# Kernel tuning notes

Measured on AMD Instinct MI355X. Metric: run time of the kernel, lower is better.

The kernel has to match this reference:

```python
import math
import jax, jax.numpy as jnp
import numpy as np

NUM_HEADS = 16


def setup_inputs() -> dict:
    key = jax.random.key(0)
    ks = jax.random.split(key, 5)
    B, S, D = 2, 2048, 1024
    return {
        "x": jax.random.normal(ks[0], (B, S, D), dtype=jnp.float32),
        "w_in": jax.random.normal(ks[1], (3 * D, D), dtype=jnp.float32) * (1.0 / math.sqrt(D)),
        "b_in": jax.random.normal(ks[2], (3 * D,), dtype=jnp.float32) * 0.02,
        "w_out": jax.random.normal(ks[3], (D, D), dtype=jnp.float32) * (1.0 / math.sqrt(D)),
        "b_out": jax.random.normal(ks[4], (D,), dtype=jnp.float32) * 0.02,
        "causal_mask": 1,
    }


def reference(x, w_in, b_in, w_out, b_out, causal_mask):
    B, S, D = x.shape
    H = NUM_HEADS
    dh = D // H
    # in-projection: torch Linear -> x @ W^T + b, then chunk into q,k,v
    qkv = x @ w_in.T + b_in                      # [B,S,3D]
    q, k, v = jnp.split(qkv, 3, axis=-1)         # each [B,S,D]
    q = q.reshape(B, S, H, dh).transpose(0, 2, 1, 3)  # [B,H,S,dh]
    k = k.reshape(B, S, H, dh).transpose(0, 2, 1, 3)
    v = v.reshape(B, S, H, dh).transpose(0, 2, 1, 3)
    # NOTE: original computes k @ q^T => scores indexed [key, query]
    scores = jnp.einsum("bhkd,bhqd->bhkq", k, q) / math.sqrt(dh)  # [B,H,Sk,Sq]
    if causal_mask:
        # triu(1) on the [k,q] matrix: mask where q_index > k_index
        mask = jnp.triu(jnp.ones((S, S), dtype=bool), 1)
        scores = jnp.where(mask, -jnp.inf, scores)
    att = jax.nn.softmax(scores, axis=-1)        # softmax over query axis (faithful)
    out = jnp.einsum("bhkq,bhqd->bhkd", att, v)  # [B,H,S,dh]
    out = out.transpose(0, 2, 1, 3).reshape(B, S, D)
    return out @ w_out.T + b_out
```

## Files before the change

kernel.cpp:

```cpp
#include <hip/hip_runtime.h>

typedef unsigned short u16;
typedef short bfrag __attribute__((ext_vector_type(8)));
typedef float facc  __attribute__((ext_vector_type(4)));
typedef float f16x  __attribute__((ext_vector_type(16)));

__device__ __forceinline__ u16 f2bf(float f){
  union { float f; unsigned u; } v; v.f = f;
  unsigned r = v.u + 0x7fffu + ((v.u >> 16) & 1u);
  return (u16)(r >> 16);
}

__device__ __forceinline__ unsigned cvt_pk_bf16(float lo, float hi){
  unsigned d;
  asm("v_cvt_pk_bf16_f32 %0, %1, %2" : "=v"(d) : "v"(lo), "v"(hi));
  return d;
}

__device__ __forceinline__ void gl_lds16(const void* g, void* l){
  __builtin_amdgcn_global_load_lds(
      (const __attribute__((address_space(1))) unsigned int*)g,
      (__attribute__((address_space(3))) unsigned int*)l,
      16, 0, 0);
}

__global__ __launch_bounds__(256) void cvt3_kernel(
    const float* __restrict__ s0, u16* __restrict__ d0, int n0,
    const float* __restrict__ s1, u16* __restrict__ d1, int n1,
    const float* __restrict__ s2, u16* __restrict__ d2)
{
  int i = (blockIdx.x * 256 + threadIdx.x) * 4;
  const float* src; u16* dst;
  if (i < n0){ src = s0; dst = d0; }
  else if (i < n0 + n1){ src = s1; dst = d1; i -= n0; }
  else { src = s2; dst = d2; i -= n0 + n1; }
  float4 f = *(const float4*)(src + i);
  ushort4 o;
  o.x = f2bf(f.x); o.y = f2bf(f.y); o.z = f2bf(f.z); o.w = f2bf(f.w);
  *(ushort4*)(dst + i) = o;
}

__device__ __forceinline__ void stage_tile(const u16* __restrict__ G, u16* lds,
                                           int row0, int k0, int K, int tid){
  #pragma unroll
  for (int c = 0; c < 2; ++c){
    int e = c * 2048 + tid * 8;
    int row = e >> 5, col = e & 31;
    gl_lds16(G + (size_t)(row0 + row) * K + k0 + col, lds + c * 2048 + (tid >> 6) * 512);
  }
}

template<int EPI>
__global__ __launch_bounds__(256) void gemm_bt(
    const u16* __restrict__ A, const u16* __restrict__ B,
    const float* __restrict__ bias, float* __restrict__ Cf,
    u16* __restrict__ qkv, int M, int N, int K)
{
  __shared__ u16 smem[16384];
  u16* Ash = smem;
  u16* Bsh = smem + 8192;
  const int tid = threadIdx.x, lane = tid & 63;
  const int w = tid >> 6, wm = w >> 1, wn = w & 1;
  const int cl = lane & 15, g8 = (lane >> 4) * 8;

  constexpr int NW = (EPI == 1) ? 12 : 4;
  const int bid = blockIdx.x;
  const int chunk = bid & 7, pos = bid >> 3;
  const int mt = (chunk >> 1) * 8 + pos / NW;
  const int nt = (chunk & 1) * NW + pos % NW;
  const int n0 = nt * 128, m0 = mt * 128;

  facc acc[4][4];
  #pragma unroll
  for (int mi = 0; mi < 4; ++mi)
    #pragma unroll
    for (int ni = 0; ni < 4; ++ni)
      acc[mi][ni] = (facc){0.f, 0.f, 0.f, 0.f};

  const int NT = K >> 5;
  stage_tile(A, Ash, m0, 0, K, tid);
  stage_tile(B, Bsh, n0, 0, K, tid);
  __syncthreads();
  int cur = 0;
  for (int kt = 0; kt < NT; ++kt){
    if (kt + 1 < NT){
      stage_tile(A, Ash + (cur ^ 1) * 4096, m0, (kt + 1) << 5, K, tid);
      stage_tile(B, Bsh + (cur ^ 1) * 4096, n0, (kt + 1) << 5, K, tid);
    }
    const u16* As = Ash + cur * 4096; const u16* Bs = Bsh + cur * 4096;
    bfrag af[4], bfr[4];
    #pragma unroll
    for (int mi = 0; mi < 4; ++mi)
      af[mi] = *(const bfrag*)&As[(wm * 64 + mi * 16 + cl) * 32 + g8];
    #pragma unroll
    for (int ni = 0; ni < 4; ++ni)
      bfr[ni] = *(const bfrag*)&Bs[(wn * 64 + ni * 16 + cl) * 32 + g8];
    #pragma unroll
    for (int mi = 0; mi < 4; ++mi)
      #pragma unroll
      for (int ni = 0; ni < 4; ++ni)
        acc[mi][ni] = __builtin_amdgcn_mfma_f32_16x16x32_bf16(af[mi], bfr[ni], acc[mi][ni], 0, 0, 0);
    __syncthreads();
    cur ^= 1;
  }

  const int r0 = (lane >> 4) * 4;
  const bool isv = (EPI == 1) && (n0 >= 2048);

  if (!isv){
    #pragma unroll
    for (int mi = 0; mi < 4; ++mi){
      const int mbase = m0 + wm * 64 + mi * 16 + r0;
      #pragma unroll
      for (int ni = 0; ni < 4; ++ni){
        const int n = n0 + wn * 64 + ni * 16 + cl;
        const float bv = bias[n];
        #pragma unroll
        for (int j = 0; j < 4; ++j){
          float v = acc[mi][ni][j] + bv;
          const int mm = mbase + j;
          if (EPI == 0){
            Cf[(size_t)mm * N + n] = v;
          } else {
            const int part = n >> 10, rest = n & 1023;
            const int h = rest >> 6, d = rest & 63;
            const int bb = mm >> 11, s = mm & 2047;
            if (part == 0) v *= 0.18033688011112042f;
            qkv[(size_t)part * 4194304 + (size_t)((bb * 16 + h) * 2048 + s) * 64 + d] = f2bf(v);
          }
        }
      }
    }
  } else {
    u16* tr = smem;
    const int bb = m0 >> 11;
    const int s0 = m0 & 2047;
    const int h0 = (n0 - 2048) >> 6;
    u16* vt_base = qkv + (size_t)2 * 4194304;
    const int trow = tid >> 2, tq = tid & 3;
    #pragma unroll
    for (int p = 0; p < 2; ++p){
      __syncthreads();
      if (wn == p){
        #pragma unroll
        for (int mi = 0; mi < 4; ++mi){
          const int sl = wm * 64 + mi * 16 + r0;
          #pragma unroll
          for (int ni = 0; ni < 4; ++ni){
            const int i = ni * 16 + cl;
            const float bv = bias[n0 + p * 64 + i];
            #pragma unroll
            for (int j = 0; j < 4; ++j)
              tr[i * 132 + sl + j] = f2bf(acc[mi][ni][j] + bv);
          }
        }
      }
      __syncthreads();
      u16* dst = vt_base + (size_t)((bb * 16 + h0 + p) * 64 + trow) * 2048 + s0 + tq * 32;
      const u16* srcr = tr + trow * 132 + tq * 32;
      #pragma unroll
      for (int k = 0; k < 4; ++k)
        *(uint4*)(dst + k * 8) = *(const uint4*)(srcr + k * 8);
    }
  }
}

template<int NSUB, bool MASK>
__device__ __forceinline__ void attn_tile(
    const u16* __restrict__ Kt, const u16* __restrict__ VTh, int jt,
    int il, int hi, const bfrag (&bq)[4],
    f16x& o0, f16x& o1, float& m_s, float& l_s)
{
  bfrag vf[NSUB * 4];
  #pragma unroll
  for (int sub = 0; sub < NSUB; ++sub)
    #pragma unroll
    for (int half = 0; half < 2; ++half){
      const int jcol = jt * 64 + sub * 32 + half * 16 + hi * 8;
      vf[sub * 4 + half * 2 + 0] = *(const bfrag*)(VTh + (size_t)il * 2048 + jcol);
      vf[sub * 4 + half * 2 + 1] = *(const bfrag*)(VTh + (size_t)(32 + il) * 2048 + jcol);
    }
  bfrag kf[NSUB * 4];
  #pragma unroll
  for (int sub = 0; sub < NSUB; ++sub)
    #pragma unroll
    for (int kt = 0; kt < 4; ++kt)
      kf[sub * 4 + kt] = *(const bfrag*)(Kt + (size_t)(sub * 32 + il) * 64 + kt * 16 + hi * 8);

  f16x s[NSUB];
  #pragma unroll
  for (int sub = 0; sub < NSUB; ++sub)
    #pragma unroll
    for (int r = 0; r < 16; ++r) s[sub][r] = 0.f;
  __builtin_amdgcn_s_setprio(1);
  #pragma unroll
  for (int kt = 0; kt < 4; ++kt)
    #pragma unroll
    for (int sub = 0; sub < NSUB; ++sub)
      s[sub] = __builtin_amdgcn_mfma_f32_32x32x16_bf16(kf[sub * 4 + kt], bq[kt], s[sub], 0, 0, 0);
  __builtin_amdgcn_s_setprio(0);

  if (MASK){
    #pragma unroll
    for (int r = 0; r < 16; ++r){
      const int qj = (r & 3) + 8 * (r >> 2) + 4 * hi;
      if (qj > il) s[NSUB - 1][r] = -1e30f;
    }
  }

  float tmax = -1e30f;
  #pragma unroll
  for (int sub = 0; sub < NSUB; ++sub){
    float a[8];
    #pragma unroll
    for (int e = 0; e < 8; ++e) a[e] = fmaxf(s[sub][e], s[sub][e + 8]);
    #pragma unroll
    for (int e = 0; e < 4; ++e) a[e] = fmaxf(a[e], a[e + 4]);
    a[0] = fmaxf(fmaxf(a[0], a[2]), fmaxf(a[1], a[3]));
    tmax = fmaxf(tmax, a[0]);
  }
  {
    auto tt = __builtin_amdgcn_permlane32_swap(__float_as_uint(tmax),
                                               __float_as_uint(tmax), false, false);
    tmax = fmaxf(__uint_as_float(tt[0]), __uint_as_float(tt[1]));
  }
  if (__any(tmax - m_s > 8.0f)){
    const float nm = fmaxf(m_s, tmax);
    const float sc = __builtin_amdgcn_exp2f(m_s - nm);
    m_s = nm; l_s *= sc;
    #pragma unroll
    for (int r = 0; r < 16; ++r){
      const float scb = __shfl(sc, (r & 3) + 8 * (r >> 2) + 4 * hi, 64);
      o0[r] *= scb; o1[r] *= scb;
    }
  }

  float rsum = 0.f;
  #pragma unroll
  for (int sub = 0; sub < NSUB; ++sub){
    #pragma unroll
    for (int r = 0; r < 16; ++r)
      s[sub][r] = __builtin_amdgcn_exp2f(s[sub][r] - m_s);
    float a[8];
    #pragma unroll
    for (int e = 0; e < 8; ++e) a[e] = s[sub][e] + s[sub][e + 8];
    #pragma unroll
    for (int e = 0; e < 4; ++e) a[e] = a[e] + a[e + 4];
    rsum += (a[0] + a[2]) + (a[1] + a[3]);
  }
  {
    auto rr = __builtin_amdgcn_permlane32_swap(__float_as_uint(rsum),
                                               __float_as_uint(rsum), false, false);
    rsum = __uint_as_float(rr[0]) + __uint_as_float(rr[1]);
  }
  l_s += rsum;

  #pragma unroll
  for (int sub = 0; sub < NSUB; ++sub)
    #pragma unroll
    for (int half = 0; half < 2; ++half){
      const int q0 = 8 * half;
      unsigned a0 = cvt_pk_bf16(s[sub][q0],     s[sub][q0 + 1]);
      unsigned a1 = cvt_pk_bf16(s[sub][q0 + 2], s[sub][q0 + 3]);
      unsigned b0 = cvt_pk_bf16(s[sub][q0 + 4], s[sub][q0 + 5]);
      unsigned b1 = cvt_pk_bf16(s[sub][q0 + 6], s[sub][q0 + 7]);
      auto r0p = __builtin_amdgcn_permlane32_swap(a0, b0, false, false);
      auto r1p = __builtin_amdgcn_permlane32_swap(a1, b1, false, false);
      union { bfrag f; unsigned u[4]; } pa;
      pa.u[0] = r0p[0]; pa.u[1] = r1p[0]; pa.u[2] = r0p[1]; pa.u[3] = r1p[1];

      __builtin_amdgcn_s_setprio(1);
      o0 = __builtin_amdgcn_mfma_f32_32x32x16_bf16(pa.f, vf[sub * 4 + half * 2 + 0], o0, 0, 0, 0);
      o1 = __builtin_amdgcn_mfma_f32_32x32x16_bf16(pa.f, vf[sub * 4 + half * 2 + 1], o1, 0, 0, 0);
      __builtin_amdgcn_s_setprio(0);
    }
}

__global__ __launch_bounds__(128, 3) void attn_kernel(
    const u16* __restrict__ qarr, const u16* __restrict__ karr,
    const u16* __restrict__ vtarr, u16* __restrict__ aout,
    const int* __restrict__ cmask)
{
  __shared__ float cO[32 * 64];
  __shared__ float cm0[32], cl0[32], cm1[32], cl1[32];
  const int tid = threadIdx.x, lane = tid & 63, w = tid >> 6;
  const int il = lane & 31, hi = lane >> 5;
  const int bh = blockIdx.x;
  const int jw = 63 - (int)blockIdx.y;
  const int iw = jw * 32;
  const u16* Qh  = karr  + (size_t)bh * 131072;
  const u16* Kh  = qarr  + (size_t)bh * 131072;
  const u16* VTh = vtarr + (size_t)bh * 131072;
  const bool do_mask = (cmask[0] != 0);

  bfrag bq[4];
  #pragma unroll
  for (int kt = 0; kt < 4; ++kt)
    bq[kt] = *(const bfrag*)(Qh + (size_t)(iw + il) * 64 + kt * 16 + hi * 8);

  f16x o0, o1;
  #pragma unroll
  for (int r = 0; r < 16; ++r){ o0[r] = 0.f; o1[r] = 0.f; }
  float m_s = -1e30f, l_s = 0.f;

  const int my_diag = jw >> 1;
  const int dsub    = jw & 1;
  const int lim = do_mask ? my_diag : 32;

  for (int jt = w; jt < lim; jt += 2)
    attn_tile<2, false>(Kh + (size_t)jt * 4096, VTh, jt, il, hi, bq, o0, o1, m_s, l_s);

  if (do_mask && (my_diag & 1) == w){
    if (dsub == 0)
      attn_tile<1, true>(Kh + (size_t)my_diag * 4096, VTh, my_diag, il, hi, bq, o0, o1, m_s, l_s);
    else
      attn_tile<2, true>(Kh + (size_t)my_diag * 4096, VTh, my_diag, il, hi, bq, o0, o1, m_s, l_s);
  }

  if (w == 1){
    #pragma unroll
    for (int r = 0; r < 16; ++r){
      const int row = (r & 3) + 8 * (r >> 2) + 4 * hi;
      cO[row * 64 + il]      = o0[r];
      cO[row * 64 + il + 32] = o1[r];
    }
    cm1[il] = m_s; cl1[il] = l_s;
  } else {
    cm0[il] = m_s; cl0[il] = l_s;
  }
  __syncthreads();
  if (w == 0){
    const int bb = bh >> 4, h = bh & 15;
    #pragma unroll
    for (int r = 0; r < 16; ++r){
      const int rl = (r & 3) + 8 * (r >> 2) + 4 * hi;
      const float mA = cm0[rl], mB = cm1[rl];
      const float lA = cl0[rl], lB = cl1[rl];
      const float M  = fmaxf(mA, mB);
      const float eA = __builtin_amdgcn_exp2f(mA - M);
      const float eB = __builtin_amdgcn_exp2f(mB - M);
      const float inv = 1.0f / (lA * eA + lB * eB);
      const float ob0 = cO[rl * 64 + il], ob1 = cO[rl * 64 + il + 32];
      u16* dst = aout + (size_t)(bb * 2048 + iw + rl) * 1024 + h * 64 + il;
      dst[0]  = f2bf((o0[r] * eA + ob0 * eB) * inv);
      dst[32] = f2bf((o1[r] * eA + ob1 * eB) * inv);
    }
  }
}

extern "C" void kernel_launch(void* const* d_in, const int* in_sizes, int n_in,
                              void* d_out, int out_size, void* d_ws, size_t ws_size,
                              hipStream_t stream)
{
  const float* x     = (const float*)d_in[0];
  const float* w_in  = (const float*)d_in[1];
  const float* b_in  = (const float*)d_in[2];
  const float* w_out = (const float*)d_in[3];
  const float* b_out = (const float*)d_in[4];
  const int*   cmask = (const int*)d_in[5];

  u16* ws     = (u16*)d_ws;
  u16* xb     = ws;
  u16* winb   = ws + 4194304;
  u16* woutb  = ws + 7340032;
  u16* qs     = ws + 8388608;
  u16* attn_o = ws + 20971520;

  cvt3_kernel<<<8192, 256, 0, stream>>>(x, xb, 4194304,
                                        w_in, winb, 3145728,
                                        w_out, woutb);

  gemm_bt<1><<<768, 256, 0, stream>>>(xb, winb, b_in, nullptr, qs, 4096, 3072, 1024);

  attn_kernel<<<dim3(32, 64), 128, 0, stream>>>(qs, qs + 4194304, qs + 8388608, attn_o, cmask);

  gemm_bt<0><<<256, 256, 0, stream>>>(attn_o, woutb, b_out, (float*)d_out, nullptr,
                                      4096, 1024, 1024);
}
```

Baseline: 148.1 us.

## Double-buffer K/V tile loads in registers with explicit vmcnt waits in attention

The non-diagonal attention loop now issues inline-asm global loads for the next K/V tile into a second register set while computing the current tile, waiting with s_waitcnt vmcnt(16) so the prefetch stays in flight. This aims to hide global memory latency behind MFMA and softmax work. The launch-bounds occupancy hint of 3 is dropped and the priority bumps are removed from the diagonal tile. Doubling the fragment registers raises VGPR pressure and may lower occupancy.

```diff
diff --git a/kernel.cpp b/kernel.cpp
--- a/kernel.cpp
+++ b/kernel.cpp
@@ -4,6 +4,7 @@
 typedef short bfrag __attribute__((ext_vector_type(8)));
 typedef float facc  __attribute__((ext_vector_type(4)));
 typedef float f16x  __attribute__((ext_vector_type(16)));
+typedef unsigned int u32x4 __attribute__((ext_vector_type(4)));
 
 __device__ __forceinline__ u16 f2bf(float f){
   union { float f; unsigned u; } v; v.f = f;
@@ -22,6 +23,25 @@
       (const __attribute__((address_space(1))) unsigned int*)g,
       (__attribute__((address_space(3))) unsigned int*)l,
       16, 0, 0);
+}
+
+__device__ __forceinline__ void gload4(u32x4& d0, u32x4& d1, u32x4& d2, u32x4& d3,
+                                       const u16* p){
+  unsigned long long a = (unsigned long long)p;
+  asm volatile("global_load_dwordx4 %0, %4, off\n\t"
+               "global_load_dwordx4 %1, %4, off offset:32\n\t"
+               "global_load_dwordx4 %2, %4, off offset:64\n\t"
+               "global_load_dwordx4 %3, %4, off offset:96"
+               : "=&v"(d0), "=&v"(d1), "=&v"(d2), "=&v"(d3)
+               : "v"(a));
+}
+__device__ __forceinline__ void wait_vm16(){
+  asm volatile("s_waitcnt vmcnt(16)" ::: "memory");
+  __builtin_amdgcn_sched_barrier(0);
+}
+__device__ __forceinline__ void wait_vm0(){
+  asm volatile("s_waitcnt vmcnt(0)" ::: "memory");
+  __builtin_amdgcn_sched_barrier(0);
 }
 
 __global__ __launch_bounds__(256) void cvt3_kernel(
@@ -165,13 +185,107 @@
   }
 }
 
-template<int NSUB, bool MASK>
-__device__ __forceinline__ void attn_tile(
+__device__ __forceinline__ void attn_compute(
+    const u32x4 (&kf)[8], const u32x4 (&vf)[8],
+    int il, int hi, const bfrag (&bq)[4],
+    f16x& o0, f16x& o1, float& m_s, float& l_s)
+{
+  f16x s0v, s1v;
+  #pragma unroll
+  for (int r = 0; r < 16; ++r){ s0v[r] = 0.f; s1v[r] = 0.f; }
+  __builtin_amdgcn_s_setprio(1);
+  #pragma unroll
+  for (int kt = 0; kt < 4; ++kt){
+    s0v = __builtin_amdgcn_mfma_f32_32x32x16_bf16(__builtin_bit_cast(bfrag, kf[kt]),     bq[kt], s0v, 0, 0, 0);
+    s1v = __builtin_amdgcn_mfma_f32_32x32x16_bf16(__builtin_bit_cast(bfrag, kf[4 + kt]), bq[kt], s1v, 0, 0, 0);
+  }
+  __builtin_amdgcn_s_setprio(0);
+
+  float tmax;
+  {
+    float a[8];
+    #pragma unroll
+    for (int e = 0; e < 8; ++e) a[e] = fmaxf(fmaxf(s0v[e], s0v[e + 8]), fmaxf(s1v[e], s1v[e + 8]));
+    #pragma unroll
+    for (int e = 0; e < 4; ++e) a[e] = fmaxf(a[e], a[e + 4]);
+    tmax = fmaxf(fmaxf(a[0], a[2]), fmaxf(a[1], a[3]));
+    auto tt = __builtin_amdgcn_permlane32_swap(__float_as_uint(tmax),
+                                               __float_as_uint(tmax), false, false);
+    tmax = fmaxf(__uint_as_float(tt[0]), __uint_as_float(tt[1]));
+  }
+  if (__any(tmax - m_s > 8.0f)){
+    const float nm = fmaxf(m_s, tmax);
+    const float sc = __builtin_amdgcn_exp2f(m_s - nm);
+    m_s = nm; l_s *= sc;
+    #pragma unroll
+    for (int r = 0; r < 16; ++r){
+      const float scb = __shfl(sc, (r & 3) + 8 * (r >> 2) + 4 * hi, 64);
+      o0[r] *= scb; o1[r] *= scb;
+    }
+  }
+
+  #pragma unroll
+  for (int r = 0; r < 16; ++r) s0v[r] = __builtin_amdgcn_exp2f(s0v[r] - m_s);
+  #pragma unroll
+  for (int r = 0; r < 16; ++r) s1v[r] = __builtin_amdgcn_exp2f(s1v[r] - m_s);
+  float rsum;
+  {
+    float a[8];
+    #pragma unroll
+    for (int e = 0; e < 8; ++e) a[e] = (s0v[e] + s0v[e + 8]) + (s1v[e] + s1v[e + 8]);
+    #pragma unroll
+    for (int e = 0; e < 4; ++e) a[e] = a[e] + a[e + 4];
+    rsum = (a[0] + a[2]) + (a[1] + a[3]);
+    auto rr = __builtin_amdgcn_permlane32_swap(__float_as_uint(rsum),
+                                               __float_as_uint(rsum), false, false);
+    rsum = __uint_as_float(rr[0]) + __uint_as_float(rr[1]);
+  }
+  l_s += rsum;
+
+  #pragma unroll
+  for (int sub = 0; sub < 2; ++sub)
+    #pragma unroll
+    for (int half = 0; half < 2; ++half){
+      const f16x& sv = sub ? s1v : s0v;
+      const int q0 = 8 * half;
+      unsigned a0 = cvt_pk_bf16(sv[q0],     sv[q0 + 1]);
+      unsigned a1 = cvt_pk_bf16(sv[q0 + 2], sv[q0 + 3]);
+      unsigned b0 = cvt_pk_bf16(sv[q0 + 4], sv[q0 + 5]);
+      unsigned b1 = cvt_pk_bf16(sv[q0 + 6], sv[q0 + 7]);
+      auto r0p = __builtin_amdgcn_permlane32_swap(a0, b0, false, false);
+      auto r1p = __builtin_amdgcn_permlane32_swap(a1, b1, false, false);
+      union { bfrag f; unsigned u[4]; } pa;
+      pa.u[0] = r0p[0]; pa.u[1] = r1p[0]; pa.u[2] = r0p[1]; pa.u[3] = r1p[1];
+
+      __builtin_amdgcn_s_setprio(1);
+      o0 = __builtin_amdgcn_mfma_f32_32x32x16_bf16(pa.f, __builtin_bit_cast(bfrag, vf[sub * 2 + half]),     o0, 0, 0, 0);
+      o1 = __builtin_amdgcn_mfma_f32_32x32x16_bf16(pa.f, __builtin_bit_cast(bfrag, vf[4 + sub * 2 + half]), o1, 0, 0, 0);
+      __builtin_amdgcn_s_setprio(0);
+    }
+}
+
+__device__ __forceinline__ void attn_issue(
+    u32x4 (&kf)[8], u32x4 (&vf)[8],
+    const u16* Kh, const u16* VTh, int jt, int il, int hi)
+{
+  const u16* k0 = Kh + (size_t)jt * 4096 + il * 64 + hi * 8;
+  const u16* k1 = k0 + 2048;
+  const u16* v0 = VTh + (size_t)il * 2048 + jt * 64 + hi * 8;
+  const u16* v1 = v0 + 32 * 2048;
+  gload4(vf[0], vf[1], vf[2], vf[3], v0);
+  gload4(vf[4], vf[5], vf[6], vf[7], v1);
+  gload4(kf[0], kf[1], kf[2], kf[3], k0);
+  gload4(kf[4], kf[5], kf[6], kf[7], k1);
+  __builtin_amdgcn_sched_barrier(0);
+}
+
+template<int NSUB>
+__device__ __forceinline__ void attn_diag(
     const u16* __restrict__ Kt, const u16* __restrict__ VTh, int jt,
     int il, int hi, const bfrag (&bq)[4],
     f16x& o0, f16x& o1, float& m_s, float& l_s)
 {
-  bfrag vf[NSUB * 4];
+  bfrag vf[NSUB * 4], kf[NSUB * 4];
   #pragma unroll
   for (int sub = 0; sub < NSUB; ++sub)
     #pragma unroll
@@ -180,7 +294,6 @@
       vf[sub * 4 + half * 2 + 0] = *(const bfrag*)(VTh + (size_t)il * 2048 + jcol);
       vf[sub * 4 + half * 2 + 1] = *(const bfrag*)(VTh + (size_t)(32 + il) * 2048 + jcol);
     }
-  bfrag kf[NSUB * 4];
   #pragma unroll
   for (int sub = 0; sub < NSUB; ++sub)
     #pragma unroll
@@ -192,20 +305,16 @@
   for (int sub = 0; sub < NSUB; ++sub)
     #pragma unroll
     for (int r = 0; r < 16; ++r) s[sub][r] = 0.f;
-  __builtin_amdgcn_s_setprio(1);
   #pragma unroll
   for (int kt = 0; kt < 4; ++kt)
     #pragma unroll
     for (int sub = 0; sub < NSUB; ++sub)
       s[sub] = __builtin_amdgcn_mfma_f32_32x32x16_bf16(kf[sub * 4 + kt], bq[kt], s[sub], 0, 0, 0);
-  __builtin_amdgcn_s_setprio(0);
-
-  if (MASK){
-    #pragma unroll
-    for (int r = 0; r < 16; ++r){
-      const int qj = (r & 3) + 8 * (r >> 2) + 4 * hi;
-      if (qj > il) s[NSUB - 1][r] = -1e30f;
-    }
+
+  #pragma unroll
+  for (int r = 0; r < 16; ++r){
+    const int qj = (r & 3) + 8 * (r >> 2) + 4 * hi;
+    if (qj > il) s[NSUB - 1][r] = -1e30f;
   }
 
   float tmax = -1e30f;
@@ -216,8 +325,7 @@
     for (int e = 0; e < 8; ++e) a[e] = fmaxf(s[sub][e], s[sub][e + 8]);
     #pragma unroll
     for (int e = 0; e < 4; ++e) a[e] = fmaxf(a[e], a[e + 4]);
-    a[0] = fmaxf(fmaxf(a[0], a[2]), fmaxf(a[1], a[3]));
-    tmax = fmaxf(tmax, a[0]);
+    tmax = fmaxf(tmax, fmaxf(fmaxf(a[0], a[2]), fmaxf(a[1], a[3])));
   }
   {
     auto tt = __builtin_amdgcn_permlane32_swap(__float_as_uint(tmax),
@@ -234,13 +342,11 @@
       o0[r] *= scb; o1[r] *= scb;
     }
   }
-
   float rsum = 0.f;
   #pragma unroll
   for (int sub = 0; sub < NSUB; ++sub){
     #pragma unroll
-    for (int r = 0; r < 16; ++r)
-      s[sub][r] = __builtin_amdgcn_exp2f(s[sub][r] - m_s);
+    for (int r = 0; r < 16; ++r) s[sub][r] = __builtin_amdgcn_exp2f(s[sub][r] - m_s);
     float a[8];
     #pragma unroll
     for (int e = 0; e < 8; ++e) a[e] = s[sub][e] + s[sub][e + 8];
@@ -268,15 +374,12 @@
       auto r1p = __builtin_amdgcn_permlane32_swap(a1, b1, false, false);
       union { bfrag f; unsigned u[4]; } pa;
       pa.u[0] = r0p[0]; pa.u[1] = r1p[0]; pa.u[2] = r0p[1]; pa.u[3] = r1p[1];
-
-      __builtin_amdgcn_s_setprio(1);
       o0 = __builtin_amdgcn_mfma_f32_32x32x16_bf16(pa.f, vf[sub * 4 + half * 2 + 0], o0, 0, 0, 0);
       o1 = __builtin_amdgcn_mfma_f32_32x32x16_bf16(pa.f, vf[sub * 4 + half * 2 + 1], o1, 0, 0, 0);
-      __builtin_amdgcn_s_setprio(0);
-    }
-}
-
-__global__ __launch_bounds__(128, 3) void attn_kernel(
+    }
+}
+
+__global__ __launch_bounds__(128) void attn_kernel(
     const u16* __restrict__ qarr, const u16* __restrict__ karr,
     const u16* __restrict__ vtarr, u16* __restrict__ aout,
     const int* __restrict__ cmask)
@@ -307,14 +410,33 @@
   const int dsub    = jw & 1;
   const int lim = do_mask ? my_diag : 32;
 
-  for (int jt = w; jt < lim; jt += 2)
-    attn_tile<2, false>(Kh + (size_t)jt * 4096, VTh, jt, il, hi, bq, o0, o1, m_s, l_s);
+  u32x4 kA[8], vA[8], kB[8], vB[8];
+  int jt = w;
+  if (jt < lim){
+    attn_issue(kA, vA, Kh, VTh, jt, il, hi);
+    while (true){
+      int nx = jt + 2;
+      bool more = nx < lim;
+      if (more) attn_issue(kB, vB, Kh, VTh, nx, il, hi);
+      if (more) wait_vm16(); else wait_vm0();
+      attn_compute(kA, vA, il, hi, bq, o0, o1, m_s, l_s);
+      jt = nx;
+      if (!more) break;
+      int nx2 = jt + 2;
+      bool more2 = nx2 < lim;
+      if (more2) attn_issue(kA, vA, Kh, VTh, nx2, il, hi);
+      if (more2) wait_vm16(); else wait_vm0();
+      attn_compute(kB, vB, il, hi, bq, o0, o1, m_s, l_s);
+      jt = nx2;
+      if (!more2) break;
+    }
+  }
 
   if (do_mask && (my_diag & 1) == w){
     if (dsub == 0)
-      attn_tile<1, true>(Kh + (size_t)my_diag * 4096, VTh, my_diag, il, hi, bq, o0, o1, m_s, l_s);
+      attn_diag<1>(Kh + (size_t)my_diag * 4096, VTh, my_diag, il, hi, bq, o0, o1, m_s, l_s);
     else
-      attn_tile<2, true>(Kh + (size_t)my_diag * 4096, VTh, my_diag, il, hi, bq, o0, o1, m_s, l_s);
+      attn_diag<2>(Kh + (size_t)my_diag * 4096, VTh, my_diag, il, hi, bq, o0, o1, m_s, l_s);
   }
 
   if (w == 1){
```

Result: no change. 148.9 us (+0.5%).

## Replace QKV projection GEMM with 256x256-tile 8-wave pipelined swizzled kernel

Applied to the files above, without the earlier changes.

The QKV in-projection GEMM moves to a new kernel with 256x256 output tiles, 512 threads (8 waves), a 4-slot LDS ring of 64-wide K stages with XOR swizzling, explicit vmcnt/lgkmcnt waits, barriers and setprio around MFMA bursts. The goal is more data reuse per loaded tile, fewer LDS bank conflicts, and overlap of global-to-LDS loads with MFMA work. The V-transpose epilogue now writes packed bf16 pairs into a larger LDS buffer in a single pass. The cost is much higher LDS usage (about 129KB per block), only 192 blocks on a 256-CU part, and hand-tuned wait counts that are fragile.

```diff
diff --git a/kernel.cpp b/kernel.cpp
--- a/kernel.cpp
+++ b/kernel.cpp
@@ -40,6 +40,212 @@
   *(ushort4*)(dst + i) = o;
 }
 
+__global__ __launch_bounds__(512, 2) void gemm8p_qkv(
+    const u16* __restrict__ A, const u16* __restrict__ B,
+    const float* __restrict__ bias, u16* __restrict__ qkv)
+{
+  __shared__ u16 lds[66048];
+  const int tid = threadIdx.x, lane = tid & 63;
+  const int w = tid >> 6, wm = w >> 2, wn = w & 3;
+  const int cl = lane & 15, g8 = (lane >> 4) * 8, r0 = (lane >> 4) * 4;
+  constexpr int K = 1024, NT = 16;
+
+  const int bid = blockIdx.x;
+  const int chunk = bid & 7, pos = bid >> 3;
+  const int mt = (chunk >> 2) * 8 + pos / 3;
+  const int nt = (chunk & 3) * 3 + pos % 3;
+  const int m0 = mt * 256, n0 = nt * 256;
+
+  facc acc[8][4];
+  #pragma unroll
+  for (int mi = 0; mi < 8; ++mi)
+    #pragma unroll
+    for (int ni = 0; ni < 4; ++ni) acc[mi][ni] = (facc){0.f, 0.f, 0.f, 0.f};
+
+  int aoff[4][2], boff[2][2];
+  #pragma unroll
+  for (int mi2 = 0; mi2 < 4; ++mi2)
+    #pragma unroll
+    for (int ks = 0; ks < 2; ++ks){
+      int r = (2 * mi2 + wm) * 16 + cl;
+      int U = r * 128 + (ks * 32 + g8) * 2;
+      aoff[mi2][ks] = (U ^ (((U >> 9) & 1) << 5)) >> 1;
+    }
+  #pragma unroll
+  for (int ni2 = 0; ni2 < 2; ++ni2)
+    #pragma unroll
+    for (int ks = 0; ks < 2; ++ks){
+      int rB = (4 * ni2 + wn) * 16 + cl;
+      int U = rB * 128 + (ks * 32 + g8) * 2;
+      boff[ni2][ks] = (U ^ (((U >> 9) & 1) << 5)) >> 1;
+    }
+
+  int srow[2], scol[2];
+  #pragma unroll
+  for (int c = 0; c < 2; ++c){
+    int Bh = c * 8192 + tid * 16;
+    int E = Bh ^ (((Bh >> 9) & 1) << 5);
+    srow[c] = E >> 7; scol[c] = (E & 127) >> 1;
+  }
+
+  auto stageA = [&](int t, int h){
+    const int k0 = (t < NT) ? t * 64 : 0;
+    const int slot = ((2 * t + h) & 3) * 8192;
+    #pragma unroll
+    for (int c = 0; c < 2; ++c)
+      gl_lds16(A + (size_t)(m0 + h * 128 + srow[c]) * K + k0 + scol[c],
+               lds + slot + c * 4096 + w * 512);
+  };
+  auto stageB = [&](int t, int h){
+    const int k0 = (t < NT) ? t * 64 : 0;
+    const int slot = 32768 + ((2 * t + h) & 3) * 8192;
+    #pragma unroll
+    for (int c = 0; c < 2; ++c)
+      gl_lds16(B + (size_t)(n0 + h * 128 + srow[c]) * K + k0 + scol[c],
+               lds + slot + c * 4096 + w * 512);
+  };
+
+  stageA(0, 0); stageB(0, 0); stageA(0, 1); stageB(0, 1); stageA(1, 0); stageB(1, 0);
+
+  bfrag af[4][2], bf[2][2];
+
+  for (int j = 0; j < NT; ++j){
+    const int sa0 = ((2 * j) & 3) * 8192,      sa1 = ((2 * j + 1) & 3) * 8192;
+    const int sb0 = 32768 + ((2 * j) & 3) * 8192, sb1 = 32768 + ((2 * j + 1) & 3) * 8192;
+
+    stageA(j + 1, 1);
+    asm volatile("s_waitcnt vmcnt(8)" ::: "memory");
+    __builtin_amdgcn_s_barrier();
+    #pragma unroll
+    for (int mi2 = 0; mi2 < 4; ++mi2)
+      #pragma unroll
+      for (int ks = 0; ks < 2; ++ks) af[mi2][ks] = *(const bfrag*)&lds[sa0 + aoff[mi2][ks]];
+    #pragma unroll
+    for (int ni2 = 0; ni2 < 2; ++ni2)
+      #pragma unroll
+      for (int ks = 0; ks < 2; ++ks) bf[ni2][ks] = *(const bfrag*)&lds[sb0 + boff[ni2][ks]];
+    asm volatile("s_waitcnt lgkmcnt(0)" ::: "memory");
+    __builtin_amdgcn_sched_barrier(0);
+    __builtin_amdgcn_s_setprio(1);
+    #pragma unroll
+    for (int mi2 = 0; mi2 < 4; ++mi2)
+      #pragma unroll
+      for (int ni2 = 0; ni2 < 2; ++ni2)
+        #pragma unroll
+        for (int ks = 0; ks < 2; ++ks)
+          acc[mi2][ni2] = __builtin_amdgcn_mfma_f32_16x16x32_bf16(af[mi2][ks], bf[ni2][ks], acc[mi2][ni2], 0, 0, 0);
+    __builtin_amdgcn_s_setprio(0);
+    __builtin_amdgcn_s_barrier();
+
+    stageB(j + 1, 1);
+    asm volatile("s_waitcnt vmcnt(6)" ::: "memory");
+    __builtin_amdgcn_s_barrier();
+    #pragma unroll
+    for (int ni2 = 0; ni2 < 2; ++ni2)
+      #pragma unroll
+      for (int ks = 0; ks < 2; ++ks) bf[ni2][ks] = *(const bfrag*)&lds[sb1 + boff[ni2][ks]];
+    asm volatile("s_waitcnt lgkmcnt(0)" ::: "memory");
+    __builtin_amdgcn_sched_barrier(0);
+    __builtin_amdgcn_s_setprio(1);
+    #pragma unroll
+    for (int mi2 = 0; mi2 < 4; ++mi2)
+      #pragma unroll
+      for (int ni2 = 0; ni2 < 2; ++ni2)
+        #pragma unroll
+        for (int ks = 0; ks < 2; ++ks)
+          acc[mi2][2 + ni2] = __builtin_amdgcn_mfma_f32_16x16x32_bf16(af[mi2][ks], bf[ni2][ks], acc[mi2][2 + ni2], 0, 0, 0);
+    __builtin_amdgcn_s_setprio(0);
+    __builtin_amdgcn_s_barrier();
+
+    #pragma unroll
+    for (int mi2 = 0; mi2 < 4; ++mi2)
+      #pragma unroll
+      for (int ks = 0; ks < 2; ++ks) af[mi2][ks] = *(const bfrag*)&lds[sa1 + aoff[mi2][ks]];
+    #pragma unroll
+    for (int ni2 = 0; ni2 < 2; ++ni2)
+      #pragma unroll
+      for (int ks = 0; ks < 2; ++ks) bf[ni2][ks] = *(const bfrag*)&lds[sb0 + boff[ni2][ks]];
+    stageA(j + 2, 0);
+    __builtin_amdgcn_s_barrier();
+    asm volatile("s_waitcnt lgkmcnt(0)" ::: "memory");
+    __builtin_amdgcn_sched_barrier(0);
+    __builtin_amdgcn_s_setprio(1);
+    #pragma unroll
+    for (int mi2 = 0; mi2 < 4; ++mi2)
+      #pragma unroll
+      for (int ni2 = 0; ni2 < 2; ++ni2)
+        #pragma unroll
+        for (int ks = 0; ks < 2; ++ks)
+          acc[4 + mi2][ni2] = __builtin_amdgcn_mfma_f32_16x16x32_bf16(af[mi2][ks], bf[ni2][ks], acc[4 + mi2][ni2], 0, 0, 0);
+    __builtin_amdgcn_s_setprio(0);
+    __builtin_amdgcn_s_barrier();
+
+    #pragma unroll
+    for (int ni2 = 0; ni2 < 2; ++ni2)
+      #pragma unroll
+      for (int ks = 0; ks < 2; ++ks) bf[ni2][ks] = *(const bfrag*)&lds[sb1 + boff[ni2][ks]];
+    stageB(j + 2, 0);
+    __builtin_amdgcn_s_barrier();
+    asm volatile("s_waitcnt lgkmcnt(0)" ::: "memory");
+    __builtin_amdgcn_sched_barrier(0);
+    __builtin_amdgcn_s_setprio(1);
+    #pragma unroll
+    for (int mi2 = 0; mi2 < 4; ++mi2)
+      #pragma unroll
+      for (int ni2 = 0; ni2 < 2; ++ni2)
+        #pragma unroll
+        for (int ks = 0; ks < 2; ++ks)
+          acc[4 + mi2][2 + ni2] = __builtin_amdgcn_mfma_f32_16x16x32_bf16(af[mi2][ks], bf[ni2][ks], acc[4 + mi2][2 + ni2], 0, 0, 0);
+    __builtin_amdgcn_s_setprio(0);
+    __builtin_amdgcn_s_barrier();
+  }
+  __syncthreads();
+
+  const int bb = m0 >> 11, s0q = m0 & 2047;
+  if (n0 < 2048){
+    #pragma unroll
+    for (int mi = 0; mi < 8; ++mi){
+      const int m = m0 + (2 * mi + wm) * 16 + r0;
+      #pragma unroll
+      for (int ni = 0; ni < 4; ++ni){
+        const int n = n0 + (4 * ni + wn) * 16 + cl;
+        const float bv = bias[n];
+        const int part = n >> 10, rest = n & 1023;
+        const int h = rest >> 6, d = rest & 63;
+        #pragma unroll
+        for (int jj = 0; jj < 4; ++jj){
+          float v = acc[mi][ni][jj] + bv;
+          if (part == 0) v *= 0.18033688011112042f;
+          const int mm = m + jj;
+          qkv[(size_t)part * 4194304 + (size_t)(((mm >> 11) * 16 + h) * 2048 + (mm & 2047)) * 64 + d] = f2bf(v);
+        }
+      }
+    }
+  } else {
+    u16* tr = lds;
+    const int h0 = (n0 - 2048) >> 6;
+    #pragma unroll
+    for (int mi = 0; mi < 8; ++mi){
+      const int sl = (2 * mi + wm) * 16 + r0;
+      #pragma unroll
+      for (int ni = 0; ni < 4; ++ni){
+        const float bv = bias[n0 + (4 * ni + wn) * 16 + cl];
+        const int off = (ni * 64 + wn * 16 + cl) * 258 + sl;
+        *(unsigned*)&tr[off]     = cvt_pk_bf16(acc[mi][ni][0] + bv, acc[mi][ni][1] + bv);
+        *(unsigned*)&tr[off + 2] = cvt_pk_bf16(acc[mi][ni][2] + bv, acc[mi][ni][3] + bv);
+      }
+    }
+    __syncthreads();
+    u16* vt_base = qkv + (size_t)2 * 4194304;
+    const int hh = tid >> 7, dd = (tid >> 1) & 63, hf = tid & 1;
+    u16* dst = vt_base + ((size_t)((bb * 16 + h0 + hh) * 64 + dd)) * 2048 + s0q + hf * 128;
+    const u16* srcr = &tr[(hh * 64 + dd) * 258 + hf * 128];
+    #pragma unroll
+    for (int k = 0; k < 16; ++k)
+      *(uint4*)(dst + k * 8) = *(const uint4*)(srcr + k * 8);
+  }
+}
+
 __device__ __forceinline__ void stage_tile(const u16* __restrict__ G, u16* lds,
                                            int row0, int k0, int K, int tid){
   #pragma unroll
@@ -50,11 +256,10 @@
   }
 }
 
-template<int EPI>
-__global__ __launch_bounds__(256) void gemm_bt(
+__global__ __launch_bounds__(256) void gemm_out(
     const u16* __restrict__ A, const u16* __restrict__ B,
     const float* __restrict__ bias, float* __restrict__ Cf,
-    u16* __restrict__ qkv, int M, int N, int K)
+    int M, int N, int K)
 {
   __shared__ u16 smem[16384];
   u16* Ash = smem;
@@ -63,11 +268,10 @@
   const int w = tid >> 6, wm = w >> 1, wn = w & 1;
   const int cl = lane & 15, g8 = (lane >> 4) * 8;
 
-  constexpr int NW = (EPI == 1) ? 12 : 4;
   const int bid = blockIdx.x;
   const int chunk = bid & 7, pos = bid >> 3;
-  const int mt = (chunk >> 1) * 8 + pos / NW;
-  const int nt = (chunk & 1) * NW + pos % NW;
+  const int mt = (chunk >> 1) * 8 + pos / 4;
+  const int nt = (chunk & 1) * 4 + pos % 4;
   const int n0 = nt * 128, m0 = mt * 128;
 
   facc acc[4][4];
@@ -105,62 +309,16 @@
   }
 
   const int r0 = (lane >> 4) * 4;
-  const bool isv = (EPI == 1) && (n0 >= 2048);
-
-  if (!isv){
-    #pragma unroll
-    for (int mi = 0; mi < 4; ++mi){
-      const int mbase = m0 + wm * 64 + mi * 16 + r0;
-      #pragma unroll
-      for (int ni = 0; ni < 4; ++ni){
-        const int n = n0 + wn * 64 + ni * 16 + cl;
-        const float bv = bias[n];
-        #pragma unroll
-        for (int j = 0; j < 4; ++j){
-          float v = acc[mi][ni][j] + bv;
-          const int mm = mbase + j;
-          if (EPI == 0){
-            Cf[(size_t)mm * N + n] = v;
-          } else {
-            const int part = n >> 10, rest = n & 1023;
-            const int h = rest >> 6, d = rest & 63;
-            const int bb = mm >> 11, s = mm & 2047;
-            if (part == 0) v *= 0.18033688011112042f;
-            qkv[(size_t)part * 4194304 + (size_t)((bb * 16 + h) * 2048 + s) * 64 + d] = f2bf(v);
-          }
-        }
-      }
-    }
-  } else {
-    u16* tr = smem;
-    const int bb = m0 >> 11;
-    const int s0 = m0 & 2047;
-    const int h0 = (n0 - 2048) >> 6;
-    u16* vt_base = qkv + (size_t)2 * 4194304;
-    const int trow = tid >> 2, tq = tid & 3;
-    #pragma unroll
-    for (int p = 0; p < 2; ++p){
-      __syncthreads();
-      if (wn == p){
-        #pragma unroll
-        for (int mi = 0; mi < 4; ++mi){
-          const int sl = wm * 64 + mi * 16 + r0;
-          #pragma unroll
-          for (int ni = 0; ni < 4; ++ni){
-            const int i = ni * 16 + cl;
-            const float bv = bias[n0 + p * 64 + i];
-            #pragma unroll
-            for (int j = 0; j < 4; ++j)
-              tr[i * 132 + sl + j] = f2bf(acc[mi][ni][j] + bv);
-          }
-        }
-      }
-      __syncthreads();
-      u16* dst = vt_base + (size_t)((bb * 16 + h0 + p) * 64 + trow) * 2048 + s0 + tq * 32;
-      const u16* srcr = tr + trow * 132 + tq * 32;
-      #pragma unroll
-      for (int k = 0; k < 4; ++k)
-        *(uint4*)(dst + k * 8) = *(const uint4*)(srcr + k * 8);
+  #pragma unroll
+  for (int mi = 0; mi < 4; ++mi){
+    const int mbase = m0 + wm * 64 + mi * 16 + r0;
+    #pragma unroll
+    for (int ni = 0; ni < 4; ++ni){
+      const int n = n0 + wn * 64 + ni * 16 + cl;
+      const float bv = bias[n];
+      #pragma unroll
+      for (int j = 0; j < 4; ++j)
+        Cf[(size_t)(mbase + j) * N + n] = acc[mi][ni][j] + bv;
     }
   }
 }
@@ -370,10 +528,10 @@
                                         w_in, winb, 3145728,
                                         w_out, woutb);
 
-  gemm_bt<1><<<768, 256, 0, stream>>>(xb, winb, b_in, nullptr, qs, 4096, 3072, 1024);
+  gemm8p_qkv<<<192, 512, 0, stream>>>(xb, winb, b_in, qs);
 
   attn_kernel<<<dim3(32, 64), 128, 0, stream>>>(qs, qs + 4194304, qs + 8388608, attn_o, cmask);
 
-  gemm_bt<0><<<256, 256, 0, stream>>>(attn_o, woutb, b_out, (float*)d_out, nullptr,
-                                      4096, 1024, 1024);
-}
+  gemm_out<<<256, 256, 0, stream>>>(attn_o, woutb, b_out, (float*)d_out,
+                                    4096, 1024, 1024);
+}
```

After: 146.9 us. No clear change (-0.8%).
